# Kernel tuning notes

Hardware: AMD Instinct MI355X
Metric: run time of the kernel (lower is better)

The kernel has to match this reference:

```python
import jax, jax.numpy as jnp
import numpy as np

NUM_BANDS = 8
NUM_CHANNELS = 16
KC = NUM_BANDS * NUM_CHANNELS
EMA_KERNEL_LENGTH = 100
DELTA = 0.1
EPS = 1e-06
S_INIT = 0.04


def setup_inputs() -> dict:
    key = jax.random.key(0)
    kx, = jax.random.split(key, 1)
    x = jax.random.normal(kx, (32, NUM_BANDS, NUM_CHANNELS, 8192), dtype=jnp.float32)
    alpha_raw = jnp.zeros((KC,), dtype=jnp.float32)
    log_s = jnp.full((KC,), float(np.log(S_INIT / (1.0 - S_INIT))), dtype=jnp.float32)
    return {"x": x, "alpha_raw": alpha_raw, "log_s": log_s}


def _build_ema_kernel(log_s):
    # (KC, 1, L_full) causal EMA kernel, then caller slices last L taps
    Lf = EMA_KERNEL_LENGTH
    s = jax.nn.sigmoid(log_s)                      # (KC,)
    j = jnp.arange(Lf, dtype=s.dtype)              # (Lf,)
    impulse = s[:, None] * (1.0 - s[:, None]) ** j[None, :]   # (KC, Lf)
    impulse = impulse / (impulse.sum(axis=1, keepdims=True) + 1e-08)
    kernel = impulse[:, ::-1]                      # flip to causal conv kernel
    return kernel[:, None, :]                      # (KC, 1, Lf)


def reference(x, alpha_raw, log_s):
    B, K, C, T = x.shape
    x_flat = x.reshape(B, KC, T)
    alpha = jax.nn.sigmoid(alpha_raw) * 0.5        # (KC,) in (0, 0.5)
    x_mag = jnp.abs(x_flat)
    L = min(EMA_KERNEL_LENGTH, T)
    kernel = _build_ema_kernel(log_s)[:, :, -L:]   # (KC, 1, L)
    x_padded = jnp.pad(x_mag, ((0, 0), (0, 0), (L - 1, 0)))
    # depthwise causal conv: groups = KC
    M = jax.lax.conv_general_dilated(
        x_padded, kernel,
        window_strides=(1,), padding='VALID',
        feature_group_count=KC,
        dimension_numbers=('NCH', 'OIH', 'NCH'))   # (B, KC, T)
    gain = jnp.clip(M, EPS, None) ** alpha[None, :, None] + DELTA
    out_flat = x_flat / gain
    return out_flat.reshape(B, K, C, T)
```

## Files before the change

### kernel.cpp

```cpp
#include <hip/hip_runtime.h>
#include <hip/hip_fp16.h>
#include <math.h>


constexpr int T      = 8192;
constexpr int KC_    = 128;
constexpr int LEN    = 100;
constexpr int BLOCK  = 256;
constexpr int CHUNK  = 32;
constexpr float EPS_   = 1e-6f;
constexpr float DELTA_ = 0.1f;
constexpr float LOG2E  = 1.4426950408889634f;

__device__ __forceinline__ int sk(int t) { return t + ((t >> 5) << 1); }

__device__ __forceinline__ float fast_sigmoid(float x) {
    const float e = __builtin_amdgcn_exp2f(-x * LOG2E);
    return __builtin_amdgcn_rcpf(1.0f + e);
}

__device__ __forceinline__ float gain_div(float xv, float M, float alpha) {
    const float Mc = fmaxf(M, EPS_);
    const float g  = __builtin_amdgcn_exp2f(alpha * __builtin_amdgcn_logf(Mc)) + DELTA_;
    return xv * __builtin_amdgcn_rcpf(g);
}

__global__ __launch_bounds__(BLOCK, 8) void agc_kernel(
    const float* __restrict__ x,
    const float* __restrict__ alpha_raw,
    const float* __restrict__ log_s,
    float* __restrict__ out)
{
    __shared__ __half lh[T + ((T >> 5) << 1)];

    const int row = blockIdx.x;
    const int kc  = row & (KC_ - 1);
    const int tid = threadIdx.x;
    const float* __restrict__ xrow = x + (size_t)row * T;
    float* __restrict__ orow       = out + (size_t)row * T;

    #pragma unroll
    for (int it = 0; it < (T / 4) / BLOCK; ++it) {
        const int i = tid + it * BLOCK;
        const float4 v = reinterpret_cast<const float4*>(xrow)[i];
        const int e = sk(i * 4);
        *reinterpret_cast<__half2*>(&lh[e])     = __float22half2_rn(make_float2(v.x, v.y));
        *reinterpret_cast<__half2*>(&lh[e + 2]) = __float22half2_rn(make_float2(v.z, v.w));
    }

    const float s     = fast_sigmoid(log_s[kc]);
    const float alpha = 0.5f * fast_sigmoid(alpha_raw[kc]);
    const float q     = 1.0f - s;
    const float q100  = __builtin_amdgcn_exp2f(100.0f * __builtin_amdgcn_logf(q));
    const float norm  = (1.0f - q100) + 1e-8f;
    const float w0    = s / norm;
    const float c3    = w0 * q100;

    __syncthreads();

    const int t0 = tid * CHUNK;

    auto ld2 = [&](int t) -> float2 {
        return __half22float2(*reinterpret_cast<const __half2*>(&lh[sk(t)]));
    };

    if (t0 >= 128) {
        float m0 = 0.0f, m1 = 0.0f;
        const float qq = q * q;
        float whi = w0 * q;
        float wlo = whi * q;
        #pragma unroll 7
        for (int i = 0; i < 49; ++i) {
            const float2 f = ld2(t0 - 2 * i - 2);
            m0 = fmaf(wlo, fabsf(f.x), m0);
            m1 = fmaf(whi, fabsf(f.y), m1);
            wlo *= qq; whi *= qq;
        }
        {
            const float2 f = ld2(t0 - LEN);
            m1 = fmaf(whi, fabsf(f.y), m1);
        }
        float M = m0 + m1;

        float o[4];
        #pragma unroll
        for (int m = 0; m < CHUNK / 2; ++m) {
            const float2 xf = ld2(t0 + 2 * m);
            const float2 xb = ld2(t0 - LEN + 2 * m);
            if (m == 0) M = fmaf(w0, fabsf(xf.x), M);
            else        M = fmaf(q, M, fmaf(w0, fabsf(xf.x), -c3 * fabsf(xb.x)));
            o[(2 * m)     & 3] = gain_div(xf.x, M, alpha);
            M = fmaf(q, M, fmaf(w0, fabsf(xf.y), -c3 * fabsf(xb.y)));
            o[(2 * m + 1) & 3] = gain_div(xf.y, M, alpha);
            if (m & 1)
                reinterpret_cast<float4*>(orow)[(t0 >> 2) + (m >> 1)] =
                    make_float4(o[0], o[1], o[2], o[3]);
        }
    } else {
        float M = 0.0f;
        float wj = w0;
        for (int j = 0; j <= t0; ++j) {
            M = fmaf(wj, fabsf((float)lh[sk(t0 - j)]), M);
            wj *= q;
        }
        float o[4];
        #pragma unroll
        for (int k = 0; k < CHUNK; ++k) {
            const int t = t0 + k;
            const float xv = (float)lh[sk(t)];
            if (k > 0) {
                const int tb = t - LEN;
                const float xb = (tb >= 0) ? fabsf((float)lh[sk(tb)]) : 0.0f;
                M = fmaf(q, M, fmaf(w0, fabsf(xv), -c3 * xb));
            }
            o[k & 3] = gain_div(xv, M, alpha);
            if ((k & 3) == 3)
                reinterpret_cast<float4*>(orow)[(t0 >> 2) + (k >> 2)] =
                    make_float4(o[0], o[1], o[2], o[3]);
        }
    }
}

extern "C" void kernel_launch(void* const* d_in, const int* in_sizes, int n_in,
                              void* d_out, int out_size, void* d_ws, size_t ws_size,
                              hipStream_t stream) {
    const float* x         = (const float*)d_in[0];
    const float* alpha_raw = (const float*)d_in[1];
    const float* log_s     = (const float*)d_in[2];
    float* out             = (float*)d_out;
    const int nrows = in_sizes[0] / T;
    agc_kernel<<<nrows, BLOCK, 0, stream>>>(x, alpha_raw, log_s, out);
}
```

Baseline: 263.2 us.

## Replace per-thread 100-tap EMA warmup with chunk partial sums shared via LDS

After: 250.4 us. 4.8% less time.

```diff
diff --git a/kernel.cpp b/kernel.cpp
--- a/kernel.cpp
+++ b/kernel.cpp
@@ -8,6 +8,8 @@
 constexpr int LEN    = 100;
 constexpr int BLOCK  = 256;
 constexpr int CHUNK  = 32;
+constexpr int PAD    = 104;
+constexpr int TP     = T + PAD;
 constexpr float EPS_   = 1e-6f;
 constexpr float DELTA_ = 0.1f;
 constexpr float LOG2E  = 1.4426950408889634f;
@@ -31,7 +33,8 @@
     const float* __restrict__ log_s,
     float* __restrict__ out)
 {
-    __shared__ __half lh[T + ((T >> 5) << 1)];
+    __shared__ __half lh[TP + ((TP >> 5) << 1)];
+    __shared__ float  Pe[BLOCK + 3];
 
     const int row = blockIdx.x;
     const int kc  = row & (KC_ - 1);
@@ -39,11 +42,16 @@
     const float* __restrict__ xrow = x + (size_t)row * T;
     float* __restrict__ orow       = out + (size_t)row * T;
 
+    if (tid < PAD / 2)
+        *reinterpret_cast<__half2*>(&lh[sk(2 * tid)]) =
+            __float22half2_rn(make_float2(0.0f, 0.0f));
+    if (tid < 3) Pe[tid] = 0.0f;
+
     #pragma unroll
     for (int it = 0; it < (T / 4) / BLOCK; ++it) {
         const int i = tid + it * BLOCK;
         const float4 v = reinterpret_cast<const float4*>(xrow)[i];
-        const int e = sk(i * 4);
+        const int e = sk(PAD + i * 4);
         *reinterpret_cast<__half2*>(&lh[e])     = __float22half2_rn(make_float2(v.x, v.y));
         *reinterpret_cast<__half2*>(&lh[e + 2]) = __float22half2_rn(make_float2(v.z, v.w));
     }
@@ -51,7 +59,11 @@
     const float s     = fast_sigmoid(log_s[kc]);
     const float alpha = 0.5f * fast_sigmoid(alpha_raw[kc]);
     const float q     = 1.0f - s;
-    const float q100  = __builtin_amdgcn_exp2f(100.0f * __builtin_amdgcn_logf(q));
+    const float lq    = __builtin_amdgcn_logf(q);
+    const float q32   = __builtin_amdgcn_exp2f(32.0f * lq);
+    const float q64   = q32 * q32;
+    const float q96   = q64 * q32;
+    const float q100  = __builtin_amdgcn_exp2f(100.0f * lq);
     const float norm  = (1.0f - q100) + 1e-8f;
     const float w0    = s / norm;
     const float c3    = w0 * q100;
@@ -61,63 +73,46 @@
     const int t0 = tid * CHUNK;
 
     auto ld2 = [&](int t) -> float2 {
-        return __half22float2(*reinterpret_cast<const __half2*>(&lh[sk(t)]));
+        return __half22float2(*reinterpret_cast<const __half2*>(&lh[sk(PAD + t)]));
     };
 
-    if (t0 >= 128) {
-        float m0 = 0.0f, m1 = 0.0f;
-        const float qq = q * q;
-        float whi = w0 * q;
-        float wlo = whi * q;
-        #pragma unroll 7
-        for (int i = 0; i < 49; ++i) {
-            const float2 f = ld2(t0 - 2 * i - 2);
-            m0 = fmaf(wlo, fabsf(f.x), m0);
-            m1 = fmaf(whi, fabsf(f.y), m1);
-            wlo *= qq; whi *= qq;
-        }
-        {
-            const float2 f = ld2(t0 - LEN);
-            m1 = fmaf(whi, fabsf(f.y), m1);
-        }
-        float M = m0 + m1;
+    __half2 h2[CHUNK / 2];
+    #pragma unroll
+    for (int i = 0; i < CHUNK / 2; ++i)
+        h2[i] = *reinterpret_cast<const __half2*>(&lh[sk(PAD + t0 + 2 * i)]);
 
-        float o[4];
-        #pragma unroll
-        for (int m = 0; m < CHUNK / 2; ++m) {
-            const float2 xf = ld2(t0 + 2 * m);
-            const float2 xb = ld2(t0 - LEN + 2 * m);
-            if (m == 0) M = fmaf(w0, fabsf(xf.x), M);
-            else        M = fmaf(q, M, fmaf(w0, fabsf(xf.x), -c3 * fabsf(xb.x)));
-            o[(2 * m)     & 3] = gain_div(xf.x, M, alpha);
-            M = fmaf(q, M, fmaf(w0, fabsf(xf.y), -c3 * fabsf(xb.y)));
-            o[(2 * m + 1) & 3] = gain_div(xf.y, M, alpha);
-            if (m & 1)
-                reinterpret_cast<float4*>(orow)[(t0 >> 2) + (m >> 1)] =
-                    make_float4(o[0], o[1], o[2], o[3]);
-        }
-    } else {
-        float M = 0.0f;
-        float wj = w0;
-        for (int j = 0; j <= t0; ++j) {
-            M = fmaf(wj, fabsf((float)lh[sk(t0 - j)]), M);
-            wj *= q;
-        }
-        float o[4];
-        #pragma unroll
-        for (int k = 0; k < CHUNK; ++k) {
-            const int t = t0 + k;
-            const float xv = (float)lh[sk(t)];
-            if (k > 0) {
-                const int tb = t - LEN;
-                const float xb = (tb >= 0) ? fabsf((float)lh[sk(tb)]) : 0.0f;
-                M = fmaf(q, M, fmaf(w0, fabsf(xv), -c3 * xb));
-            }
-            o[k & 3] = gain_div(xv, M, alpha);
-            if ((k & 3) == 3)
-                reinterpret_cast<float4*>(orow)[(t0 >> 2) + (k >> 2)] =
-                    make_float4(o[0], o[1], o[2], o[3]);
-        }
+    float P = 0.0f;
+    const float qq = q * q;
+    #pragma unroll
+    for (int i = 0; i < CHUNK / 2; ++i) {
+        const float2 f = __half22float2(h2[i]);
+        P = fmaf(qq, P, fmaf(q, fabsf(f.x), fabsf(f.y)));
+    }
+    Pe[3 + tid] = P;
+    __syncthreads();
+
+    const float2 pA = ld2(t0 - 100);
+    const float2 pB = ld2(t0 - 98);
+    float corr = fmaf(q, fabsf(pA.x), fabsf(pA.y));
+    corr = fmaf(q, corr, fabsf(pB.x));
+    corr = fmaf(q, corr, fabsf(pB.y));
+    float h = fmaf(q32, Pe[1 + tid], Pe[2 + tid]);
+    h = fmaf(q64, Pe[tid], h);
+    h = fmaf(q96, corr, h);
+    float M = w0 * h;
+
+    float o[4];
+    #pragma unroll
+    for (int m = 0; m < CHUNK / 2; ++m) {
+        const float2 xf = __half22float2(h2[m]);
+        const float2 xb = ld2(t0 - LEN + 2 * m);
+        M = fmaf(q, M, fmaf(w0, fabsf(xf.x), -c3 * fabsf(xb.x)));
+        o[(2 * m)     & 3] = gain_div(xf.x, M, alpha);
+        M = fmaf(q, M, fmaf(w0, fabsf(xf.y), -c3 * fabsf(xb.y)));
+        o[(2 * m + 1) & 3] = gain_div(xf.y, M, alpha);
+        if (m & 1)
+            reinterpret_cast<float4*>(orow)[(t0 >> 2) + (m >> 1)] =
+                make_float4(o[0], o[1], o[2], o[3]);
     }
 }
 
```
